# Performance work log

Hardware: AMD Instinct MI355X
Metric: run time of the kernel (lower is better)

## Reference

```python
import jax, jax.numpy as jnp
import numpy as np

B, M, FIN = 16, 49152, 16
F1, K = 32, 5
NNZ = 8 * M  # ~8 neighbors per vertex on a HEALPix sphere mesh


def setup_inputs() -> dict:
    key = jax.random.key(0)
    kx, kr, kc, kv, kw, kb = jax.random.split(key, 6)
    x = jax.random.normal(kx, (B, M, FIN), dtype=jnp.float32)
    rows = jax.random.randint(kr, (NNZ,), 0, M, dtype=jnp.int32)
    cols = jax.random.randint(kc, (NNZ,), 0, M, dtype=jnp.int32)
    # small values keep the order-K Chebyshev recurrence numerically tame
    vals = jax.random.normal(kv, (NNZ,), dtype=jnp.float32) * 0.1
    stddev = 1.0 / np.sqrt(FIN * (K + 0.5) / 2.0)
    kernel = jax.random.normal(kw, (FIN * K, F1), dtype=jnp.float32) * stddev
    bias = jax.random.uniform(kb, (1, 1, F1), dtype=jnp.float32) * 0.05
    return {"x": x, "rows": rows, "cols": cols, "vals": vals,
            "kernel": kernel, "bias": bias}


def reference(x, rows, cols, vals, kernel, bias):
    # x: [B, M, Fin]; sparse Laplacian L in COO (rows, cols, vals), shape [M, M]
    b, m, fin = x.shape
    k = kernel.shape[0] // fin

    def spmm(X):  # L @ X for X: [M, Fin*B]
        return jax.ops.segment_sum(vals[:, None] * X[cols], rows, num_segments=m)

    # x0: [M, Fin*B] exactly as the TF transpose/reshape does
    x0 = jnp.transpose(x, (1, 2, 0)).reshape(m, fin * b)
    xs = [x0]
    if k > 1:
        x1 = spmm(x0)
        xs.append(x1)
    for _ in range(2, k):
        x2 = 2.0 * spmm(x1) - x0
        xs.append(x2)
        x0, x1 = x1, x2
    # [K, M, Fin, B] -> [B, M, Fin, K] -> [B*M, Fin*K]
    xk = jnp.stack(xs, axis=0).reshape(k, m, fin, b)
    xk = jnp.transpose(xk, (3, 1, 2, 0)).reshape(b * m, fin * k)
    out = (xk @ kernel).reshape(b, m, -1)  # [B, M, F1]
    return out + bias
```

## Files before the change

kernel.cpp:

```cpp
#include <hip/hip_runtime.h>


constexpr int M   = 49152;
constexpr int B   = 16;
constexpr int FIN = 16;
constexpr int F1  = 32;
constexpr int K   = 5;
constexpr int XBS = M * FIN;
constexpr size_t SLICEB   = (size_t)M * 64;
constexpr size_t BUFBYTES = (size_t)M * 512;
constexpr int NBLK_M = M / 256;
constexpr int NHB = 64 * NBLK_M;

typedef short s16x8 __attribute__((ext_vector_type(8)));
typedef float f32x4 __attribute__((ext_vector_type(4)));
typedef unsigned int u32;
typedef unsigned long long u64;
typedef u32 u32x4 __attribute__((ext_vector_type(4)));

#define DEVFN __device__ __forceinline__

DEVFN float lo2f(u32 d) {
  union { u32 u; float f; } v; v.u = d << 16; return v.f;
}
DEVFN float hi2f(u32 d) {
  union { u32 u; float f; } v; v.u = d & 0xffff0000u; return v.f;
}
DEVFN unsigned short f2bf(float f) {
  union { float f; u32 u; } v;
  v.f = f;
  u32 r = (v.u + 0x7FFFu + ((v.u >> 16) & 1u)) >> 16;
  return (unsigned short)r;
}


__global__ __launch_bounds__(256) void transform_x(const float* __restrict__ x,
                                                   char* __restrict__ x0b) {
  int lane = threadIdx.x & 63, wave = threadIdx.x >> 6;
  int mchunk = blockIdx.x >> 2, bquad = blockIdx.x & 3;
  int b = bquad * 4 + wave;
  int m = mchunk * 16 + (lane >> 2);
  int f = (lane & 3) * 4;
  float4 v = *(const float4*)(x + (size_t)b * XBS + (size_t)m * FIN + f);
  ushort4 r = make_ushort4(f2bf(v.x), f2bf(v.y), f2bf(v.z), f2bf(v.w));
  *(ushort4*)(x0b + (size_t)(b >> 1) * SLICEB + (size_t)m * 64 +
              (size_t)(b & 1) * 32 + (size_t)(lane & 3) * 8) = r;
}


__global__ __launch_bounds__(256) void hist_kernel(const int* __restrict__ rows,
                                                   int* __restrict__ counts, int nnz) {
  int i = blockIdx.x * 256 + threadIdx.x;
  if (i < nnz) atomicAdd(&counts[rows[i]], 1);
}

DEVFN int wave_incl_scan(int v, int lane) {
#pragma unroll
  for (int off = 1; off < 64; off <<= 1) {
    int t = __shfl_up(v, off);
    if (lane >= off) v += t;
  }
  return v;
}

__global__ __launch_bounds__(1024) void scan_blocks(const int* __restrict__ src,
                                                    int* __restrict__ dst,
                                                    int* __restrict__ partials) {
  __shared__ int wsum[16];
  int tid = threadIdx.x, lane = tid & 63, w = tid >> 6;
  int i = blockIdx.x * 1024 + tid;
  int s = wave_incl_scan(src[i], lane);
  if (lane == 63) wsum[w] = s;
  __syncthreads();
  if (tid < 16) {
    int t = wsum[tid];
#pragma unroll
    for (int off = 1; off < 16; off <<= 1) {
      int u = __shfl_up(t, off);
      if (tid >= off) t += u;
    }
    wsum[tid] = t;
  }
  __syncthreads();
  int base = (w > 0) ? wsum[w - 1] : 0;
  s += base;
  dst[i + 1] = s;
  if (tid == 1023) partials[blockIdx.x] = s;
}

__global__ void scan_partials_kernel(int* __restrict__ partials,
                                     int* __restrict__ dst, int nblk) {
  int lane = threadIdx.x;
  int v = (lane < nblk) ? partials[lane] : 0;
  v = wave_incl_scan(v, lane);
  if (lane < nblk) partials[lane] = v;
  if (lane == 0) dst[0] = 0;
}

__global__ __launch_bounds__(1024) void scan_add_kernel(int* __restrict__ dst,
                                                        const int* __restrict__ partials) {
  if (blockIdx.x == 0) return;
  int i = blockIdx.x * 1024 + threadIdx.x;
  dst[i + 1] += partials[blockIdx.x - 1];
}

__global__ __launch_bounds__(256) void scatter_kernel(const int* __restrict__ rows,
                                                      const int* __restrict__ cols,
                                                      const float* __restrict__ vals,
                                                      const int* __restrict__ row_ptr8,
                                                      int* __restrict__ fill,
                                                      u32* __restrict__ cvp, int nnz) {
  int i = blockIdx.x * 256 + threadIdx.x;
  if (i < nnz) {
    int r = rows[i];
    int pos = row_ptr8[r] + atomicAdd(&fill[r], 1);
    cvp[pos] = ((u32)cols[i] << 16) | (u32)f2bf(vals[i]);
  }
}


__global__ __launch_bounds__(256) void deg_hist_blk(const int* __restrict__ counts,
                                                    int* __restrict__ c8,
                                                    int* __restrict__ blkhist) {
  __shared__ int lh[64];
  int tid = threadIdx.x;
  if (tid < 64) lh[tid] = 0;
  __syncthreads();
  int m = blockIdx.x * 256 + tid;
  int d = counts[m];
  c8[m] = (d + 8) & ~7;
  atomicAdd(&lh[min(d, 63)], 1);
  __syncthreads();
  if (tid < 64) blkhist[tid * NBLK_M + blockIdx.x] = lh[tid];
}

__global__ __launch_bounds__(256) void perm_scatter_blk(const int* __restrict__ counts,
                                                        const int* __restrict__ sc,
                                                        int* __restrict__ perm) {
  __shared__ int lh[64];
  __shared__ int lbase[64];
  int tid = threadIdx.x, blk = blockIdx.x;
  if (tid < 64) lh[tid] = 0;
  __syncthreads();
  int m = blk * 256 + tid;
  int d = min(counts[m], 63);
  int lr = atomicAdd(&lh[d], 1);
  __syncthreads();
  if (tid < 64) lbase[tid] = sc[tid * NBLK_M + blk];
  __syncthreads();
  perm[lbase[d] + lr] = m;
}


template <bool SUB>
__global__ __launch_bounds__(256) void spmm_pad16(const char* __restrict__ xsrc,
                                                  const char* __restrict__ ssrc,
                                                  char* __restrict__ y,
                                                  const int* __restrict__ row_ptr8,
                                                  const int* __restrict__ perm,
                                                  const u32* __restrict__ cvp) {
  int s  = blockIdx.x & 7;
  int g4 = blockIdx.x >> 3;
  int lane = threadIdx.x & 63, wave = threadIdx.x >> 6;
  int r = lane >> 2, q2 = lane & 3;
  int grp = g4 * 4 + wave;
  const char* sbase = xsrc + (size_t)s * SLICEB;
  size_t qb = (size_t)q2 * 16;

  int rid  = perm[grp * 16 + r];
  int base = row_ptr8[rid];
  int plim = row_ptr8[rid + 1] - base - 1;

  int wns = (plim + 1) >> 3;
  wns = max(wns, __shfl_xor(wns, 4));
  wns = max(wns, __shfl_xor(wns, 8));
  wns = max(wns, __shfl_xor(wns, 16));
  wns = max(wns, __shfl_xor(wns, 32));

  u64 sv0 = 0, sv1 = 0;
  if (SUB) {
    const char* sp = ssrc + (size_t)s * SLICEB + (size_t)rid * 64 + qb;
    sv0 = __builtin_nontemporal_load((const u64*)sp);
    sv1 = __builtin_nontemporal_load((const u64*)(sp + 8));
  }

  float a0 = 0.f, a1 = 0.f, a2 = 0.f, a3 = 0.f;
  float a4 = 0.f, a5 = 0.f, a6 = 0.f, a7 = 0.f;
  int nedge = wns * 8;
  for (int t0 = 0; t0 < nedge; t0 += 8) {
    u32 cA[8];
    u32x4 dA[8];
#pragma unroll
    for (int t = 0; t < 8; ++t) cA[t] = cvp[base + min(t0 + t, plim)];
#pragma unroll
    for (int t = 0; t < 8; ++t)
      dA[t] = *(const u32x4*)(sbase + (size_t)(cA[t] >> 16) * 64 + qb);
#pragma unroll
    for (int t = 0; t < 8; ++t) {
      float v = lo2f(cA[t]);
      a0 = fmaf(v, lo2f(dA[t].x), a0); a1 = fmaf(v, hi2f(dA[t].x), a1);
      a2 = fmaf(v, lo2f(dA[t].y), a2); a3 = fmaf(v, hi2f(dA[t].y), a3);
      a4 = fmaf(v, lo2f(dA[t].z), a4); a5 = fmaf(v, hi2f(dA[t].z), a5);
      a6 = fmaf(v, lo2f(dA[t].w), a6); a7 = fmaf(v, hi2f(dA[t].w), a7);
    }
  }

  if (SUB) {
    u32 s0 = (u32)sv0, s1 = (u32)(sv0 >> 32);
    u32 s2 = (u32)sv1, s3 = (u32)(sv1 >> 32);
    a0 = fmaf(2.f, a0, -lo2f(s0)); a1 = fmaf(2.f, a1, -hi2f(s0));
    a2 = fmaf(2.f, a2, -lo2f(s1)); a3 = fmaf(2.f, a3, -hi2f(s1));
    a4 = fmaf(2.f, a4, -lo2f(s2)); a5 = fmaf(2.f, a5, -hi2f(s2));
    a6 = fmaf(2.f, a6, -lo2f(s3)); a7 = fmaf(2.f, a7, -hi2f(s3));
  }
  u64 rv0 = ((u64)(((u32)f2bf(a3) << 16) | (u32)f2bf(a2)) << 32) |
            (u64)(((u32)f2bf(a1) << 16) | (u32)f2bf(a0));
  u64 rv1 = ((u64)(((u32)f2bf(a7) << 16) | (u32)f2bf(a6)) << 32) |
            (u64)(((u32)f2bf(a5) << 16) | (u32)f2bf(a4));
  char* yp = y + (size_t)s * SLICEB + (size_t)rid * 64 + qb;
  __builtin_nontemporal_store(rv0, (u64*)yp);
  __builtin_nontemporal_store(rv1, (u64*)(yp + 8));
}


__global__ __launch_bounds__(256) void cheb_gemm_mfma(const char* __restrict__ xs0,
                                                      const float* __restrict__ kern,
                                                      const float* __restrict__ bias,
                                                      float* __restrict__ out) {
  __shared__ unsigned short bl[3][4][32][8];
  __shared__ float bsl[32];
  int tid = threadIdx.x;
  for (int idx = tid; idx < 3 * 4 * 32 * 8; idx += 256) {
    int j = idx & 7, o = (idx >> 3) & 31, g = (idx >> 8) & 3, c = idx >> 10;
    int k = 2 * c + (g >> 1), f = (g & 1) * 8 + j;
    bl[c][g][o][j] = (k < K) ? f2bf(kern[(f * K + k) * F1 + o]) : (unsigned short)0;
  }
  if (tid < 32) bsl[tid] = bias[tid];
  __syncthreads();

  int lane = tid & 63, wave = tid >> 6;
  int pair = blockIdx.x & 7;
  int bb = wave & 1;
  int mtg = (blockIdx.x >> 3) * 2 + (wave >> 1);
  int b = pair * 2 + bb;
  int mt0 = mtg * 8;

  int row = lane & 15, g = lane >> 4;
  int col = lane & 15;

  s16x8 bf[3][2];
#pragma unroll
  for (int c = 0; c < 3; ++c) {
#pragma unroll
    for (int ot = 0; ot < 2; ++ot)
      bf[c][ot] = *(const s16x8*)(&bl[c][g][2 * col + ot][0]);
  }
  float bias0 = bsl[2 * col], bias1 = bsl[2 * col + 1];

  size_t lanebyte = (size_t)pair * SLICEB + (size_t)row * 64 +
                    (size_t)bb * 32 + (size_t)(g & 1) * 16;
  int khalf = g >> 1;
  const char* p0 = xs0 + (size_t)(0 + khalf) * BUFBYTES + lanebyte;
  const char* p1 = xs0 + (size_t)(2 + khalf) * BUFBYTES + lanebyte;
  const char* p2 = xs0 + (size_t)(4 + khalf) * BUFBYTES + lanebyte;

  size_t obase0 = ((size_t)b * M + (size_t)mt0 * 16) * F1;

#pragma unroll 2
  for (int t = 0; t < 8; ++t) {
    size_t moff = (size_t)(mt0 + t) * (16 * 64);
    s16x8 a0 = *(const s16x8*)(p0 + moff);
    s16x8 a1 = *(const s16x8*)(p1 + moff);
    s16x8 a2 = (g < 2) ? *(const s16x8*)(p2 + moff) : (s16x8)0;

    f32x4 acc0 = {0.f, 0.f, 0.f, 0.f};
    f32x4 acc1 = {0.f, 0.f, 0.f, 0.f};
    acc0 = __builtin_amdgcn_mfma_f32_16x16x32_bf16(a0, bf[0][0], acc0, 0, 0, 0);
    acc1 = __builtin_amdgcn_mfma_f32_16x16x32_bf16(a0, bf[0][1], acc1, 0, 0, 0);
    acc0 = __builtin_amdgcn_mfma_f32_16x16x32_bf16(a1, bf[1][0], acc0, 0, 0, 0);
    acc1 = __builtin_amdgcn_mfma_f32_16x16x32_bf16(a1, bf[1][1], acc1, 0, 0, 0);
    acc0 = __builtin_amdgcn_mfma_f32_16x16x32_bf16(a2, bf[2][0], acc0, 0, 0, 0);
    acc1 = __builtin_amdgcn_mfma_f32_16x16x32_bf16(a2, bf[2][1], acc1, 0, 0, 0);

    float* ob = out + obase0 + (size_t)t * (16 * F1);
#pragma unroll
    for (int j = 0; j < 4; ++j) {
      int r = g * 4 + j;
      float2 st = make_float2(acc0[j] + bias0, acc1[j] + bias1);
      *(float2*)(ob + r * F1 + 2 * col) = st;
    }
  }
}


extern "C" void kernel_launch(void* const* d_in, const int* in_sizes, int n_in,
                              void* d_out, int out_size, void* d_ws, size_t ws_size,
                              hipStream_t stream) {
  const float* x    = (const float*)d_in[0];
  const int*   rows = (const int*)d_in[1];
  const int*   cols = (const int*)d_in[2];
  const float* vals = (const float*)d_in[3];
  const float* kern = (const float*)d_in[4];
  const float* bias = (const float*)d_in[5];
  float* out = (float*)d_out;
  int nnz = in_sizes[1];
  int padWords = nnz + 8 * M + 256;

  char* x0b = (char*)d_ws;
  char* x1b = x0b + BUFBYTES;
  char* x2b = x1b + BUFBYTES;
  char* x3b = x2b + BUFBYTES;
  char* x4b = x3b + BUFBYTES;
  int* row_ptr8 = (int*)(x4b + BUFBYTES);
  int* counts   = row_ptr8 + (M + 256);
  int* fill     = counts + M;
  int* c8       = fill + M;
  int* partials = c8 + M;
  int* blkhist  = partials + 256;
  int* sc       = blkhist + NHB;
  int* perm     = sc + NHB + 256;
  u32* cvp8     = (u32*)(perm + M);

  int nblk1024 = M / 1024;
  int nblkH    = NHB / 1024;
  int nblkNnz  = (nnz + 255) / 256;

  transform_x<<<(M / 16) * 4, 256, 0, stream>>>(x, x0b);

  hipMemsetAsync(counts, 0, (size_t)2 * M * 4, stream);
  hipMemsetAsync(cvp8, 0, (size_t)padWords * 4, stream);
  hist_kernel<<<nblkNnz, 256, 0, stream>>>(rows, counts, nnz);
  deg_hist_blk<<<NBLK_M, 256, 0, stream>>>(counts, c8, blkhist);
  scan_blocks<<<nblk1024, 1024, 0, stream>>>(c8, row_ptr8, partials);
  scan_partials_kernel<<<1, 64, 0, stream>>>(partials, row_ptr8, nblk1024);
  scan_add_kernel<<<nblk1024, 1024, 0, stream>>>(row_ptr8, partials);
  scan_blocks<<<nblkH, 1024, 0, stream>>>(blkhist, sc, partials);
  scan_partials_kernel<<<1, 64, 0, stream>>>(partials, sc, nblkH);
  scan_add_kernel<<<nblkH, 1024, 0, stream>>>(sc, partials);
  perm_scatter_blk<<<NBLK_M, 256, 0, stream>>>(counts, sc, perm);
  scatter_kernel<<<nblkNnz, 256, 0, stream>>>(rows, cols, vals, row_ptr8, fill, cvp8, nnz);

  int spmmGrid = 8 * (M / 64);
  spmm_pad16<false><<<spmmGrid, 256, 0, stream>>>(x0b, nullptr, x1b, row_ptr8, perm, cvp8);
  spmm_pad16<true ><<<spmmGrid, 256, 0, stream>>>(x1b, x0b, x2b, row_ptr8, perm, cvp8);
  spmm_pad16<true ><<<spmmGrid, 256, 0, stream>>>(x2b, x1b, x3b, row_ptr8, perm, cvp8);
  spmm_pad16<true ><<<spmmGrid, 256, 0, stream>>>(x3b, x2b, x4b, row_ptr8, perm, cvp8);

  cheb_gemm_mfma<<<1536, 256, 0, stream>>>(x0b, kern, bias, out);

  (void)n_in; (void)out_size; (void)ws_size; (void)in_sizes;
}
```

Before: 282.9 us.

## Fuse final SpMM into MFMA GEMM and merge the two prefix scans

The last Chebyshev SpMM step now runs inside the output GEMM kernel. Each wave computes x4 for its 16 rows into shared memory and feeds it straight to the MFMA, so the x4 buffer is never written to or read back from global memory. The degree-padded counts and the per-block degree histogram are also concatenated into one array, so a single three-kernel scan replaces two. In exchange, the fused kernel drops the degree-sorted row permutation for its SpMM part, which may worsen load balance. The GEMM also now works on small per-wave tiles instead of looping over 8 tiles per wave.

Measured after the change: 261.4 us. 1.08x faster.

```diff
diff --git a/kernel.cpp b/kernel.cpp
--- a/kernel.cpp
+++ b/kernel.cpp
@@ -11,6 +11,7 @@
 constexpr size_t BUFBYTES = (size_t)M * 512;
 constexpr int NBLK_M = M / 256;
 constexpr int NHB = 64 * NBLK_M;
+constexpr int NCAT = M + NHB;
 
 typedef short s16x8 __attribute__((ext_vector_type(8)));
 typedef float f32x4 __attribute__((ext_vector_type(4)));
@@ -31,6 +32,9 @@
   v.f = f;
   u32 r = (v.u + 0x7FFFu + ((v.u >> 16) & 1u)) >> 16;
   return (unsigned short)r;
+}
+DEVFN u32 pack2(float lo, float hi) {
+  return ((u32)f2bf(hi) << 16) | (u32)f2bf(lo);
 }
 
 
@@ -120,18 +124,17 @@
 
 
 __global__ __launch_bounds__(256) void deg_hist_blk(const int* __restrict__ counts,
-                                                    int* __restrict__ c8,
-                                                    int* __restrict__ blkhist) {
+                                                    int* __restrict__ cc) {
   __shared__ int lh[64];
   int tid = threadIdx.x;
   if (tid < 64) lh[tid] = 0;
   __syncthreads();
   int m = blockIdx.x * 256 + tid;
   int d = counts[m];
-  c8[m] = (d + 8) & ~7;
+  cc[m] = (d + 8) & ~7;
   atomicAdd(&lh[min(d, 63)], 1);
   __syncthreads();
-  if (tid < 64) blkhist[tid * NBLK_M + blockIdx.x] = lh[tid];
+  if (tid < 64) cc[M + tid * NBLK_M + blockIdx.x] = lh[tid];
 }
 
 __global__ __launch_bounds__(256) void perm_scatter_blk(const int* __restrict__ counts,
@@ -145,8 +148,9 @@
   int m = blk * 256 + tid;
   int d = min(counts[m], 63);
   int lr = atomicAdd(&lh[d], 1);
-  __syncthreads();
-  if (tid < 64) lbase[tid] = sc[tid * NBLK_M + blk];
+  int sc0 = sc[0];
+  __syncthreads();
+  if (tid < 64) lbase[tid] = sc[tid * NBLK_M + blk] - sc0;
   __syncthreads();
   perm[lbase[d] + lr] = m;
 }
@@ -213,22 +217,25 @@
     a4 = fmaf(2.f, a4, -lo2f(s2)); a5 = fmaf(2.f, a5, -hi2f(s2));
     a6 = fmaf(2.f, a6, -lo2f(s3)); a7 = fmaf(2.f, a7, -hi2f(s3));
   }
-  u64 rv0 = ((u64)(((u32)f2bf(a3) << 16) | (u32)f2bf(a2)) << 32) |
-            (u64)(((u32)f2bf(a1) << 16) | (u32)f2bf(a0));
-  u64 rv1 = ((u64)(((u32)f2bf(a7) << 16) | (u32)f2bf(a6)) << 32) |
-            (u64)(((u32)f2bf(a5) << 16) | (u32)f2bf(a4));
+  u64 rv0 = ((u64)pack2(a2, a3) << 32) | (u64)pack2(a0, a1);
+  u64 rv1 = ((u64)pack2(a6, a7) << 32) | (u64)pack2(a4, a5);
   char* yp = y + (size_t)s * SLICEB + (size_t)rid * 64 + qb;
   __builtin_nontemporal_store(rv0, (u64*)yp);
   __builtin_nontemporal_store(rv1, (u64*)(yp + 8));
 }
 
 
-__global__ __launch_bounds__(256) void cheb_gemm_mfma(const char* __restrict__ xs0,
-                                                      const float* __restrict__ kern,
-                                                      const float* __restrict__ bias,
-                                                      float* __restrict__ out) {
+__global__ __launch_bounds__(256) void spmm_gemm_fused(const char* __restrict__ xsrc,
+                                                       const char* __restrict__ ssrc,
+                                                       const char* __restrict__ xs0,
+                                                       const float* __restrict__ kern,
+                                                       const float* __restrict__ bias,
+                                                       const int* __restrict__ row_ptr8,
+                                                       const u32* __restrict__ cvp,
+                                                       float* __restrict__ out) {
   __shared__ unsigned short bl[3][4][32][8];
   __shared__ float bsl[32];
+  __shared__ u32 x4t[4][16][16];
   int tid = threadIdx.x;
   for (int idx = tid; idx < 3 * 4 * 32 * 8; idx += 256) {
     int j = idx & 7, o = (idx >> 3) & 31, g = (idx >> 8) & 3, c = idx >> 10;
@@ -236,58 +243,103 @@
     bl[c][g][o][j] = (k < K) ? f2bf(kern[(f * K + k) * F1 + o]) : (unsigned short)0;
   }
   if (tid < 32) bsl[tid] = bias[tid];
-  __syncthreads();
-
+
+  int s  = blockIdx.x & 7;
+  int rg = blockIdx.x >> 3;
   int lane = tid & 63, wave = tid >> 6;
-  int pair = blockIdx.x & 7;
-  int bb = wave & 1;
-  int mtg = (blockIdx.x >> 3) * 2 + (wave >> 1);
-  int b = pair * 2 + bb;
-  int mt0 = mtg * 8;
+  int m0w = rg * 64 + wave * 16;
+
+  {
+    int r = lane >> 2, q2 = lane & 3;
+    int rid = m0w + r;
+    const char* sbase = xsrc + (size_t)s * SLICEB;
+    size_t qb = (size_t)q2 * 16;
+    int base = row_ptr8[rid];
+    int plim = row_ptr8[rid + 1] - base - 1;
+    int wns = (plim + 1) >> 3;
+    wns = max(wns, __shfl_xor(wns, 4));
+    wns = max(wns, __shfl_xor(wns, 8));
+    wns = max(wns, __shfl_xor(wns, 16));
+    wns = max(wns, __shfl_xor(wns, 32));
+
+    const char* sp = ssrc + (size_t)s * SLICEB + (size_t)rid * 64 + qb;
+    u64 sv0 = __builtin_nontemporal_load((const u64*)sp);
+    u64 sv1 = __builtin_nontemporal_load((const u64*)(sp + 8));
+
+    float a0 = 0.f, a1 = 0.f, a2 = 0.f, a3 = 0.f;
+    float a4 = 0.f, a5 = 0.f, a6 = 0.f, a7 = 0.f;
+    int nedge = wns * 8;
+    for (int t0 = 0; t0 < nedge; t0 += 8) {
+      u32 cA[8];
+      u32x4 dA[8];
+#pragma unroll
+      for (int t = 0; t < 8; ++t) cA[t] = cvp[base + min(t0 + t, plim)];
+#pragma unroll
+      for (int t = 0; t < 8; ++t)
+        dA[t] = *(const u32x4*)(sbase + (size_t)(cA[t] >> 16) * 64 + qb);
+#pragma unroll
+      for (int t = 0; t < 8; ++t) {
+        float v = lo2f(cA[t]);
+        a0 = fmaf(v, lo2f(dA[t].x), a0); a1 = fmaf(v, hi2f(dA[t].x), a1);
+        a2 = fmaf(v, lo2f(dA[t].y), a2); a3 = fmaf(v, hi2f(dA[t].y), a3);
+        a4 = fmaf(v, lo2f(dA[t].z), a4); a5 = fmaf(v, hi2f(dA[t].z), a5);
+        a6 = fmaf(v, lo2f(dA[t].w), a6); a7 = fmaf(v, hi2f(dA[t].w), a7);
+      }
+    }
+    u32 s0 = (u32)sv0, s1 = (u32)(sv0 >> 32);
+    u32 s2 = (u32)sv1, s3 = (u32)(sv1 >> 32);
+    a0 = fmaf(2.f, a0, -lo2f(s0)); a1 = fmaf(2.f, a1, -hi2f(s0));
+    a2 = fmaf(2.f, a2, -lo2f(s1)); a3 = fmaf(2.f, a3, -hi2f(s1));
+    a4 = fmaf(2.f, a4, -lo2f(s2)); a5 = fmaf(2.f, a5, -hi2f(s2));
+    a6 = fmaf(2.f, a6, -lo2f(s3)); a7 = fmaf(2.f, a7, -hi2f(s3));
+
+    x4t[wave][r][q2 * 4 + 0] = pack2(a0, a1);
+    x4t[wave][r][q2 * 4 + 1] = pack2(a2, a3);
+    x4t[wave][r][q2 * 4 + 2] = pack2(a4, a5);
+    x4t[wave][r][q2 * 4 + 3] = pack2(a6, a7);
+  }
+  __syncthreads();
 
   int row = lane & 15, g = lane >> 4;
-  int col = lane & 15;
-
-  s16x8 bf[3][2];
+  int col = row;
+
+  s16x8 bf_[3][2];
 #pragma unroll
   for (int c = 0; c < 3; ++c) {
 #pragma unroll
     for (int ot = 0; ot < 2; ++ot)
-      bf[c][ot] = *(const s16x8*)(&bl[c][g][2 * col + ot][0]);
+      bf_[c][ot] = *(const s16x8*)(&bl[c][g][2 * col + ot][0]);
   }
   float bias0 = bsl[2 * col], bias1 = bsl[2 * col + 1];
 
-  size_t lanebyte = (size_t)pair * SLICEB + (size_t)row * 64 +
-                    (size_t)bb * 32 + (size_t)(g & 1) * 16;
+  size_t rowbyte = (size_t)s * SLICEB + (size_t)(m0w + row) * 64 +
+                   (size_t)(g & 1) * 16;
   int khalf = g >> 1;
-  const char* p0 = xs0 + (size_t)(0 + khalf) * BUFBYTES + lanebyte;
-  const char* p1 = xs0 + (size_t)(2 + khalf) * BUFBYTES + lanebyte;
-  const char* p2 = xs0 + (size_t)(4 + khalf) * BUFBYTES + lanebyte;
-
-  size_t obase0 = ((size_t)b * M + (size_t)mt0 * 16) * F1;
-
-#pragma unroll 2
-  for (int t = 0; t < 8; ++t) {
-    size_t moff = (size_t)(mt0 + t) * (16 * 64);
-    s16x8 a0 = *(const s16x8*)(p0 + moff);
-    s16x8 a1 = *(const s16x8*)(p1 + moff);
-    s16x8 a2 = (g < 2) ? *(const s16x8*)(p2 + moff) : (s16x8)0;
+  const char* pc0 = xs0 + (size_t)khalf * BUFBYTES + rowbyte;
+  const char* pc1 = xs0 + (size_t)(2 + khalf) * BUFBYTES + rowbyte;
+
+#pragma unroll
+  for (int bb = 0; bb < 2; ++bb) {
+    s16x8 A0 = *(const s16x8*)(pc0 + bb * 32);
+    s16x8 A1 = *(const s16x8*)(pc1 + bb * 32);
+    s16x8 A2 = (g < 2) ? *(const s16x8*)(&x4t[wave][row][bb * 8 + (g & 1) * 4])
+                       : (s16x8)0;
 
     f32x4 acc0 = {0.f, 0.f, 0.f, 0.f};
     f32x4 acc1 = {0.f, 0.f, 0.f, 0.f};
-    acc0 = __builtin_amdgcn_mfma_f32_16x16x32_bf16(a0, bf[0][0], acc0, 0, 0, 0);
-    acc1 = __builtin_amdgcn_mfma_f32_16x16x32_bf16(a0, bf[0][1], acc1, 0, 0, 0);
-    acc0 = __builtin_amdgcn_mfma_f32_16x16x32_bf16(a1, bf[1][0], acc0, 0, 0, 0);
-    acc1 = __builtin_amdgcn_mfma_f32_16x16x32_bf16(a1, bf[1][1], acc1, 0, 0, 0);
-    acc0 = __builtin_amdgcn_mfma_f32_16x16x32_bf16(a2, bf[2][0], acc0, 0, 0, 0);
-    acc1 = __builtin_amdgcn_mfma_f32_16x16x32_bf16(a2, bf[2][1], acc1, 0, 0, 0);
-
-    float* ob = out + obase0 + (size_t)t * (16 * F1);
+    acc0 = __builtin_amdgcn_mfma_f32_16x16x32_bf16(A0, bf_[0][0], acc0, 0, 0, 0);
+    acc1 = __builtin_amdgcn_mfma_f32_16x16x32_bf16(A0, bf_[0][1], acc1, 0, 0, 0);
+    acc0 = __builtin_amdgcn_mfma_f32_16x16x32_bf16(A1, bf_[1][0], acc0, 0, 0, 0);
+    acc1 = __builtin_amdgcn_mfma_f32_16x16x32_bf16(A1, bf_[1][1], acc1, 0, 0, 0);
+    acc0 = __builtin_amdgcn_mfma_f32_16x16x32_bf16(A2, bf_[2][0], acc0, 0, 0, 0);
+    acc1 = __builtin_amdgcn_mfma_f32_16x16x32_bf16(A2, bf_[2][1], acc1, 0, 0, 0);
+
+    size_t ob = ((size_t)(2 * s + bb) * M + m0w) * F1;
 #pragma unroll
     for (int j = 0; j < 4; ++j) {
-      int r = g * 4 + j;
+      int crow = g * 4 + j;
       float2 st = make_float2(acc0[j] + bias0, acc1[j] + bias1);
-      *(float2*)(ob + r * F1 + 2 * col) = st;
+      *(float2*)(out + ob + (size_t)crow * F1 + 2 * col) = st;
     }
   }
 }
@@ -310,43 +362,37 @@
   char* x1b = x0b + BUFBYTES;
   char* x2b = x1b + BUFBYTES;
   char* x3b = x2b + BUFBYTES;
-  char* x4b = x3b + BUFBYTES;
-  int* row_ptr8 = (int*)(x4b + BUFBYTES);
-  int* counts   = row_ptr8 + (M + 256);
+  int* counts   = (int*)(x3b + BUFBYTES);
   int* fill     = counts + M;
-  int* c8       = fill + M;
-  int* partials = c8 + M;
-  int* blkhist  = partials + 256;
-  int* sc       = blkhist + NHB;
-  int* perm     = sc + NHB + 256;
+  int* cc       = fill + M;
+  int* D        = cc + NCAT;
+  int* partials = D + NCAT + 256;
+  int* perm     = partials + 256;
   u32* cvp8     = (u32*)(perm + M);
-
-  int nblk1024 = M / 1024;
-  int nblkH    = NHB / 1024;
-  int nblkNnz  = (nnz + 255) / 256;
+  int* sc       = D + M;
+
+  int nblkCat = NCAT / 1024;
+  int nblkNnz = (nnz + 255) / 256;
 
   transform_x<<<(M / 16) * 4, 256, 0, stream>>>(x, x0b);
 
   hipMemsetAsync(counts, 0, (size_t)2 * M * 4, stream);
   hipMemsetAsync(cvp8, 0, (size_t)padWords * 4, stream);
   hist_kernel<<<nblkNnz, 256, 0, stream>>>(rows, counts, nnz);
-  deg_hist_blk<<<NBLK_M, 256, 0, stream>>>(counts, c8, blkhist);
-  scan_blocks<<<nblk1024, 1024, 0, stream>>>(c8, row_ptr8, partials);
-  scan_partials_kernel<<<1, 64, 0, stream>>>(partials, row_ptr8, nblk1024);
-  scan_add_kernel<<<nblk1024, 1024, 0, stream>>>(row_ptr8, partials);
-  scan_blocks<<<nblkH, 1024, 0, stream>>>(blkhist, sc, partials);
-  scan_partials_kernel<<<1, 64, 0, stream>>>(partials, sc, nblkH);
-  scan_add_kernel<<<nblkH, 1024, 0, stream>>>(sc, partials);
+  deg_hist_blk<<<NBLK_M, 256, 0, stream>>>(counts, cc);
+  scan_blocks<<<nblkCat, 1024, 0, stream>>>(cc, D, partials);
+  scan_partials_kernel<<<1, 64, 0, stream>>>(partials, D, nblkCat);
+  scan_add_kernel<<<nblkCat, 1024, 0, stream>>>(D, partials);
   perm_scatter_blk<<<NBLK_M, 256, 0, stream>>>(counts, sc, perm);
-  scatter_kernel<<<nblkNnz, 256, 0, stream>>>(rows, cols, vals, row_ptr8, fill, cvp8, nnz);
+  scatter_kernel<<<nblkNnz, 256, 0, stream>>>(rows, cols, vals, D, fill, cvp8, nnz);
 
   int spmmGrid = 8 * (M / 64);
-  spmm_pad16<false><<<spmmGrid, 256, 0, stream>>>(x0b, nullptr, x1b, row_ptr8, perm, cvp8);
-  spmm_pad16<true ><<<spmmGrid, 256, 0, stream>>>(x1b, x0b, x2b, row_ptr8, perm, cvp8);
-  spmm_pad16<true ><<<spmmGrid, 256, 0, stream>>>(x2b, x1b, x3b, row_ptr8, perm, cvp8);
-  spmm_pad16<true ><<<spmmGrid, 256, 0, stream>>>(x3b, x2b, x4b, row_ptr8, perm, cvp8);
-
-  cheb_gemm_mfma<<<1536, 256, 0, stream>>>(x0b, kern, bias, out);
+  spmm_pad16<false><<<spmmGrid, 256, 0, stream>>>(x0b, nullptr, x1b, D, perm, cvp8);
+  spmm_pad16<true ><<<spmmGrid, 256, 0, stream>>>(x1b, x0b, x2b, D, perm, cvp8);
+  spmm_pad16<true ><<<spmmGrid, 256, 0, stream>>>(x2b, x1b, x3b, D, perm, cvp8);
+
+  spmm_gemm_fused<<<spmmGrid, 256, 0, stream>>>(x3b, x2b, x0b, kern, bias, D,
+                                                cvp8, out);
 
   (void)n_in; (void)out_size; (void)ws_size; (void)in_sizes;
 }
```
